# Kernel tuning notes

Measured on AMD Instinct MI355X. Metric: run time of the kernel, lower is better.

The kernel has to match this reference:

```python
import jax, jax.numpy as jnp
import numpy as np

CONF_THRES = 0.3    # from call site: non_max_suppression(pred[0], 0.3)
IOU_THRES = 0.45    # yolov5 default
MAX_NMS = 1000      # candidates entering pairwise NMS
MAX_DET = 300       # padded output detections per image
MAX_WH = 4096.0     # class-offset trick for per-class NMS


def xywh2xyxy(b):
    xy, wh = b[..., :2], b[..., 2:4]
    return jnp.concatenate([xy - wh * 0.5, xy + wh * 0.5], axis=-1)


def box_iou(a, b):
    # a: [K,4], b: [K,4] in xyxy -> iou [K,K]
    area_a = (a[:, 2] - a[:, 0]) * (a[:, 3] - a[:, 1])
    area_b = (b[:, 2] - b[:, 0]) * (b[:, 3] - b[:, 1])
    lt = jnp.maximum(a[:, None, :2], b[None, :, :2])
    rb = jnp.minimum(a[:, None, 2:], b[None, :, 2:])
    wh = jnp.clip(rb - lt, 0.0)
    inter = wh[..., 0] * wh[..., 1]
    return inter / (area_a[:, None] + area_b[None, :] - inter + 1e-7)


def _nms_single(p):
    # p: [N, 5+nc]  (xywh, obj, class scores)
    boxes = xywh2xyxy(p[:, :4])                       # [N,4]
    obj = p[:, 4]
    cls_conf = p[:, 5:] * obj[:, None]                # obj * cls
    cls = jnp.argmax(cls_conf, axis=-1)               # [N] int
    score = jnp.max(cls_conf, axis=-1)                 # [N]
    valid = (obj > CONF_THRES) & (score > CONF_THRES)
    s = jnp.where(valid, score, -jnp.inf)
    top_s, idx = jax.lax.top_k(s, MAX_NMS)            # sorted desc
    b = boxes[idx]                                     # [K,4]
    c = cls[idx]                                       # [K]
    v = top_s > -jnp.inf                               # [K] candidate mask
    # per-class NMS: shift boxes by class id so different classes never overlap
    ob = b + (c.astype(b.dtype) * MAX_WH)[:, None]
    iou = box_iou(ob, ob)                              # [K,K]

    def step(keep, xs):
        i, row = xs
        suppressed = jnp.any(keep & (row > IOU_THRES))
        ki = v[i] & ~suppressed
        return keep.at[i].set(ki), ki

    keep0 = jnp.zeros(MAX_NMS, dtype=bool)
    _, keep = jax.lax.scan(step, keep0, (jnp.arange(MAX_NMS), iou))

    # gather kept detections (score-ordered), pad to MAX_DET
    kscore = jnp.where(keep, top_s, -jnp.inf)
    det_s, det_i = jax.lax.top_k(kscore, MAX_DET)
    det_valid = (det_s > -jnp.inf)[:, None]
    det = jnp.concatenate(
        [b[det_i],                                  # xyxy
         top_s[det_i][:, None],                     # score
         c[det_i].astype(b.dtype)[:, None]],        # class
        axis=-1)                                    # [MAX_DET, 6]
    return jnp.where(det_valid, det, 0.0)


def setup_inputs() -> dict:
    key = jax.random.key(0)
    k1, k2, k3, k4 = jax.random.split(key, 4)
    B, N, NC = 16, 25200, 80
    xy = jax.random.uniform(k1, (B, N, 2), jnp.float32) * 640.0
    wh = jax.random.uniform(k2, (B, N, 2), jnp.float32) * 120.0 + 4.0
    obj = jax.random.uniform(k3, (B, N, 1), jnp.float32)
    cls = jax.random.uniform(k4, (B, N, NC), jnp.float32)
    pred = jnp.concatenate([xy, wh, obj, cls], axis=-1)  # [B,N,85]
    return {"pred": pred}


def reference(pred) -> jnp.ndarray:
    # pred: [B, N, 5+nc] -> detections [B, MAX_DET, 6] (xyxy, conf, cls), zero-padded
    return jax.vmap(_nms_single)(pred)
```

## Files before the change

### kernel.cpp

```cpp
#include <hip/hip_runtime.h>
#include <cstdint>

typedef unsigned int u32;
typedef unsigned long long u64;

#define N_BATCH 16
#define N_ROWS  25200
#define N_FEAT  85
#define N_CLS   80
#define MAX_NMS 1000
#define MAX_DET 300
#define KEY_INVALID 0xFF800000u

#define WS_KEYS    0u
#define WS_CLS     1612800u
#define WS_SELBOX  3225600u
#define WS_SELOB   3487744u
#define WS_SELAREA 3749888u
#define WS_SELSC   3815424u
#define WS_SELCLS  3880960u
#define WS_SELVAL  3946496u
#define WS_GMASK   4012032u

__device__ __forceinline__ u32 score_key(float s) {
  u32 u = __float_as_uint(s);
  u32 o = (u & 0x80000000u) ? ~u : (u | 0x80000000u);
  return ~o;
}

__device__ __forceinline__ u64 shfl_xor_u64(u64 x, int m) {
  u32 lo = (u32)x, hi = (u32)(x >> 32);
  lo = __shfl_xor(lo, m); hi = __shfl_xor(hi, m);
  return ((u64)hi << 32) | lo;
}
__device__ __forceinline__ u64 readlane_u64(u64 x, int lane) {
  u32 lo = (u32)x, hi = (u32)(x >> 32);
  u32 rlo = (u32)__builtin_amdgcn_readlane((int)lo, lane);
  u32 rhi = (u32)__builtin_amdgcn_readlane((int)hi, lane);
  return ((u64)rhi << 32) | rlo;
}

#define KS_CHUNK  32
#define KS_CBYTES (KS_CHUNK * N_FEAT * 4)
#define KS_GRID   1792
#define KS_NCHUNK ((N_BATCH * N_ROWS) / KS_CHUNK)

__device__ __forceinline__ void ks_stage(const float* pred, int c, u32* lbuf,
                                         int wv, int lane) {
  const char* g = (const char*)pred + (size_t)c * KS_CBYTES;
  const int u0 = wv * 170;
  u32* l0 = lbuf + u0 * 4;
  __builtin_amdgcn_global_load_lds(
      (const __attribute__((address_space(1))) u32*)(g + (size_t)(u0 + lane) * 16),
      (__attribute__((address_space(3))) u32*)(l0), 16, 0, 0);
  __builtin_amdgcn_global_load_lds(
      (const __attribute__((address_space(1))) u32*)(g + (size_t)(u0 + 64 + lane) * 16),
      (__attribute__((address_space(3))) u32*)(l0 + 256), 16, 0, 0);
  if (lane < 42)
    __builtin_amdgcn_global_load_lds(
        (const __attribute__((address_space(1))) u32*)(g + (size_t)(u0 + 128 + lane) * 16),
        (__attribute__((address_space(3))) u32*)(l0 + 512), 16, 0, 0);
}

__global__ __launch_bounds__(256) void k_score(const float* __restrict__ pred,
                                               u32* __restrict__ keys,
                                               u32* __restrict__ clsArr) {
  __shared__ __align__(16) u32 sbuf[2][KS_CBYTES / 4];
  const int t = threadIdx.x;
  const int lane = t & 63;
  const int wv = t >> 6;
  const int row = (lane >> 3) + wv * 8;
  const int sub = lane & 7;

  ks_stage(pred, blockIdx.x, sbuf[0], wv, lane);
  ks_stage(pred, blockIdx.x + KS_GRID, sbuf[1], wv, lane);

  int it = 0;
  for (int c = blockIdx.x; c < KS_NCHUNK; c += KS_GRID, ++it) {
    const bool has_next = (c + KS_GRID < KS_NCHUNK);
    if (has_next) asm volatile("s_waitcnt vmcnt(3)" ::: "memory");
    else          asm volatile("s_waitcnt vmcnt(0)" ::: "memory");
    __builtin_amdgcn_sched_barrier(0);
    __builtin_amdgcn_s_barrier();

    const u32* rp = sbuf[it & 1] + row * N_FEAT;
    float obj = __uint_as_float(rp[4]);
    float best = -__builtin_inff();
    int bi = 0;
    const u32* cp = rp + 5 + sub * 10;
    #pragma unroll
    for (int k = 0; k < 10; ++k) {
      float cc = __uint_as_float(cp[k]) * obj;
      if (cc > best) { best = cc; bi = sub * 10 + k; }
    }
    #pragma unroll
    for (int d = 1; d <= 4; d <<= 1) {
      float ob = __shfl_xor(best, d);
      int oj = __shfl_xor(bi, d);
      if (ob > best || (ob == best && oj < bi)) { best = ob; bi = oj; }
    }
    if (sub == 0) {
      bool valid = (obj > 0.3f) && (best > 0.3f);
      float s = valid ? best : -__builtin_inff();
      int gr = c * KS_CHUNK + row;
      keys[gr] = score_key(s);
      clsArr[gr] = (u32)bi;
    }
    __builtin_amdgcn_s_barrier();
    if (c + 2 * KS_GRID < KS_NCHUNK)
      ks_stage(pred, c + 2 * KS_GRID, sbuf[it & 1], wv, lane);
  }
}

#define RPT 25
__global__ __launch_bounds__(1024) void k_select(const float* __restrict__ pred,
    const u32* __restrict__ keys_g, const u32* __restrict__ cls_g,
    float* __restrict__ selBox, float* __restrict__ selOb, float* __restrict__ selArea,
    float* __restrict__ selScore, float* __restrict__ selCls, u32* __restrict__ selValid) {
  extern __shared__ char smem[];
  u32* skeys = (u32*)smem;
  u32* hist  = (u32*)(smem + 102400);
  u32* wsum  = (u32*)(smem + 103424);
  u32* bc    = (u32*)(smem + 103552);
  u64* items = (u64*)(smem + 103584);

  const int b = blockIdx.x;
  const int t = threadIdx.x;
  const int lane = t & 63;
  const int wv = t >> 6;

  {
    uint4* k4 = (uint4*)skeys;
    const uint4* g4 = (const uint4*)(keys_g + b * N_ROWS);
    for (int i = t; i < N_ROWS / 4; i += 1024) k4[i] = g4[i];
  }
  items[t] = 0xFFFFFFFF00000000ull | (u32)t;
  if (t == 0) { bc[0] = 0u; bc[1] = 999u; }
  __syncthreads();

  u32 rk[RPT];
  const int i0 = t * RPT;
  #pragma unroll
  for (int r = 0; r < RPT; ++r) {
    u32 k = skeys[i0 + r];
    rk[r] = (i0 + r < N_ROWS) ? k : 0xFFFFFFFFu;
  }

  for (int lev = 3; lev >= 0; --lev) {
    if (t < 256) hist[t] = 0u;
    __syncthreads();
    const u32 prefix = bc[0];
    const u32 target = bc[1];
    const int sh = lev * 8;
    if (lev == 3) {
      #pragma unroll
      for (int r = 0; r < RPT; ++r) {
        u32 bk = rk[r] >> 24;
        u64 act = __ballot(true);
        while (act) {
          int ldr = __ffsll((unsigned long long)act) - 1;
          u32 lb = __shfl(bk, ldr);
          u64 same = __ballot(bk == lb);
          if (lane == ldr) atomicAdd(&hist[lb], (u32)__popcll(same));
          act &= ~same;
        }
      }
    } else {
      const u32 maskhi = 0xFFFFFFFFu << ((lev + 1) * 8);
      #pragma unroll
      for (int r = 0; r < RPT; ++r) {
        if ((rk[r] & maskhi) == prefix)
          atomicAdd(&hist[(rk[r] >> sh) & 255u], 1u);
      }
    }
    __syncthreads();
    if (t < 64) {
      u32 c0 = hist[t*4], c1 = hist[t*4+1], c2 = hist[t*4+2], c3 = hist[t*4+3];
      u32 s4 = c0 + c1 + c2 + c3;
      u32 inc = s4;
      #pragma unroll
      for (int d = 1; d < 64; d <<= 1) { u32 o = __shfl_up(inc, d); if (lane >= d) inc += o; }
      u32 excl = inc - s4;
      u64 mb = __ballot(inc > target);
      int L = __ffsll((unsigned long long)mb) - 1;
      if (t == L) {
        u32 cum = excl; u32 d = (u32)t * 4u;
        if (cum + c0 <= target) { cum += c0; d++;
          if (cum + c1 <= target) { cum += c1; d++;
            if (cum + c2 <= target) { cum += c2; d++; } } }
        bc[0] = prefix | (d << sh);
        bc[1] = target - cum;
      }
    }
    __syncthreads();
  }
  const u32 T = bc[0];

  u32 c0 = 0, c1 = 0;
  #pragma unroll
  for (int r = 0; r < RPT; ++r) { c0 += (rk[r] < T); c1 += (rk[r] == T); }
  u32 packed = (c0 << 16) | c1;
  u32 inc = packed;
  #pragma unroll
  for (int d = 1; d < 64; d <<= 1) { u32 o = __shfl_up(inc, d); if (lane >= d) inc += o; }
  if (lane == 63) wsum[wv] = inc;
  __syncthreads();
  if (t < 16) {
    u32 v = wsum[t]; u32 iv = v;
    #pragma unroll
    for (int d = 1; d < 16; d <<= 1) { u32 o = __shfl_up(iv, d); if (lane >= d) iv += o; }
    wsum[t] = iv - v;
    if (t == 15) bc[2] = iv;
  }
  __syncthreads();
  u32 excl = inc - packed + wsum[wv];
  u32 total0 = bc[2] >> 16;
  u32 p0 = excl >> 16;
  u32 p1 = total0 + (excl & 0xFFFFu);
  #pragma unroll
  for (int r = 0; r < RPT; ++r) {
    u32 k = rk[r];
    if (k < T)       { items[p0] = ((u64)k << 32) | (u32)(i0 + r); p0++; }
    else if (k == T) { if (p1 < (u32)MAX_NMS) items[p1] = ((u64)k << 32) | (u32)(i0 + r); p1++; }
  }
  __syncthreads();

  u64 v = items[t];
  #pragma unroll
  for (int k = 2; k <= 64; k <<= 1) {
    for (int j = k >> 1; j > 0; j >>= 1) {
      u64 p = shfl_xor_u64(v, j);
      bool keepmin = (((t & k) == 0) == ((t & j) == 0));
      v = (keepmin == (v < p)) ? v : p;
    }
  }
  for (int k = 128; k <= 1024; k <<= 1) {
    for (int j = k >> 1; j >= 64; j >>= 1) {
      items[t] = v;
      __syncthreads();
      u64 p = items[t ^ j];
      bool keepmin = (((t & k) == 0) == ((t & j) == 0));
      v = (keepmin == (v < p)) ? v : p;
      __syncthreads();
    }
    #pragma unroll
    for (int j = 32; j > 0; j >>= 1) {
      u64 p = shfl_xor_u64(v, j);
      bool keepmin = (((t & k) == 0) == ((t & j) == 0));
      v = (keepmin == (v < p)) ? v : p;
    }
  }

  if (t < MAX_NMS) {
    u64 it = v;
    u32 key = (u32)(it >> 32);
    u32 row = (u32)(it & 0xFFFFFFFFu);
    u32 o = ~key;
    u32 sb = (o & 0x80000000u) ? (o ^ 0x80000000u) : ~o;
    float score = __uint_as_float(sb);
    u32 valid = (key != KEY_INVALID) ? 1u : 0u;
    const float* p = pred + ((size_t)b * N_ROWS + row) * N_FEAT;
    float x = p[0], y = p[1], w = p[2], h = p[3];
    float x1 = x - w * 0.5f, y1 = y - h * 0.5f;
    float x2 = x + w * 0.5f, y2 = y + h * 0.5f;
    float cf = (float)cls_g[b * N_ROWS + row];
    float offv = cf * 4096.0f;
    float o0 = x1 + offv, o1 = y1 + offv, o2 = x2 + offv, o3 = y2 + offv;
    float area = (o2 - o0) * (o3 - o1);
    int idx = b * 1024 + t;
    selBox[idx * 4 + 0] = x1; selBox[idx * 4 + 1] = y1;
    selBox[idx * 4 + 2] = x2; selBox[idx * 4 + 3] = y2;
    selOb [idx * 4 + 0] = o0; selOb [idx * 4 + 1] = o1;
    selOb [idx * 4 + 2] = o2; selOb [idx * 4 + 3] = o3;
    selArea[idx] = area;
    selScore[idx] = score;
    selCls[idx] = cf;
    selValid[idx] = valid;
  }
}

__global__ __launch_bounds__(256) void k_mask(const float* __restrict__ selOb,
                                              const float* __restrict__ selArea,
                                              u64* __restrict__ gmask) {
  __shared__ float shob[1024 * 4];
  __shared__ float sharea[1024];
  const int chunk = blockIdx.x;
  const int b = blockIdx.y;
  const int t = threadIdx.x;
  const int lane = t & 63;
  const int wv = t >> 6;
  {
    float4* so4 = (float4*)shob;
    const float4* go4 = (const float4*)(selOb + (size_t)b * 4096);
    for (int i = t; i < 1024; i += 256) so4[i] = go4[i];
    float4* sa4 = (float4*)sharea;
    const float4* ga4 = (const float4*)(selArea + (size_t)b * 1024);
    if (t < 256) sa4[t] = ga4[t];
  }
  __syncthreads();
  const float4* job = (const float4*)shob;
  for (int k = 0; k < 8; ++k) {
    int i = chunk * 32 + wv * 8 + k;
    if (i >= MAX_NMS) break;
    float a0 = shob[i*4+0], a1 = shob[i*4+1], a2 = shob[i*4+2], a3 = shob[i*4+3];
    float aa = sharea[i];
    for (int w = (i >> 6); w < 16; ++w) {
      int j = w * 64 + lane;
      float4 bb = job[j];
      float aj = sharea[j];
      float lt0 = fmaxf(a0, bb.x);
      float lt1 = fmaxf(a1, bb.y);
      float rb0 = fminf(a2, bb.z);
      float rb1 = fminf(a3, bb.w);
      float ww = fmaxf(rb0 - lt0, 0.0f);
      float hh = fmaxf(rb1 - lt1, 0.0f);
      float inter = ww * hh;
      float den = aa + aj - inter + 1e-7f;
      float iou = inter / den;
      u64 bits = __ballot(iou > 0.45f);
      if (lane == 0) gmask[((size_t)b * MAX_NMS + i) * 16 + w] = bits;
    }
  }
}

__global__ __launch_bounds__(256) void k_scan(const u64* __restrict__ gmask,
                                              const u32* __restrict__ selValid,
                                              const float* __restrict__ selBox,
                                              const float* __restrict__ selScore,
                                              const float* __restrict__ selCls,
                                              float* __restrict__ out) {
  extern __shared__ char smem[];
  u64* m = (u64*)smem;
  u64* aw = (u64*)(smem + 128000);
  int* order = (int*)(smem + 128128);
  u32* pcnt = (u32*)(smem + 129328);
  const int b = blockIdx.x;
  const int t = threadIdx.x;
  const int lane = t & 63;
  const int wv = t >> 6;

  {
    const char* g = (const char*)(gmask + (size_t)b * (MAX_NMS * 16));
    for (int u = wv; u < 125; u += 4) {
      __builtin_amdgcn_global_load_lds(
          (const __attribute__((address_space(1))) u32*)(g + (size_t)u * 1024 + (size_t)lane * 16),
          (__attribute__((address_space(3))) u32*)((u32*)m + u * 256), 16, 0, 0);
    }
  }
  for (int s = t; s < 1024; s += 256) {
    u32 vv = (s < MAX_NMS) ? selValid[b * 1024 + s] : 0u;
    u64 bal = __ballot(vv != 0u);
    if ((s & 63) == 0) aw[s >> 6] = bal;
  }
  asm volatile("s_waitcnt vmcnt(0)" ::: "memory");
  __syncthreads();

  if (t < 64) {
    u64 A = (t < 16) ? aw[t] : 0ull;
    int cnt = 0;
    for (int w0 = 0; w0 < 16 && cnt < MAX_DET; ++w0) {
      u64 Aw = readlane_u64(A, w0);
      if (Aw == 0ull) continue;
      int myrow = w0 * 64 + t;
      u64 dm = (myrow < MAX_NMS) ? m[myrow * 16 + w0] : 0ull;
      u32 dml = (u32)dm, dmh = (u32)(dm >> 32);
      u64 keepw = 0ull;
      const int cnt0 = cnt;
      while (Aw != 0ull && cnt < MAX_DET) {
        int bit = __ffsll((unsigned long long)Aw) - 1;
        keepw |= (1ull << bit);
        ++cnt;
        u64 sup = ((u64)(u32)__builtin_amdgcn_readlane((int)dmh, bit) << 32)
                |        (u32)__builtin_amdgcn_readlane((int)dml, bit);
        Aw &= ~sup;
        Aw &= ~(1ull << bit);
      }
      if ((keepw >> t) & 1ull) {
        int rank = (int)__popcll(keepw & ((1ull << t) - 1ull));
        order[cnt0 + rank] = w0 * 64 + t;
      }
      if (cnt >= MAX_DET) break;
      u64 kk = keepw;
      const u64* mr = m + (size_t)w0 * 64 * 16;
      while (kk != 0ull) {
        int b0 = __ffsll((unsigned long long)kk) - 1; kk &= kk - 1;
        int b1 = b0, b2 = b0, b3 = b0;
        if (kk) { b1 = __ffsll((unsigned long long)kk) - 1; kk &= kk - 1;
          if (kk) { b2 = __ffsll((unsigned long long)kk) - 1; kk &= kk - 1;
            if (kk) { b3 = __ffsll((unsigned long long)kk) - 1; kk &= kk - 1; } } }
        if (t < 16) {
          u64 r0 = mr[b0 * 16 + t];
          u64 r1 = mr[b1 * 16 + t];
          u64 r2 = mr[b2 * 16 + t];
          u64 r3 = mr[b3 * 16 + t];
          A &= ~(r0 | r1 | r2 | r3);
        }
      }
    }
    if (t == 0) *pcnt = (u32)cnt;
  }
  __syncthreads();
  int cnt = (int)*pcnt;
  for (int s = t; s < MAX_DET; s += 256) {
    float o0=0,o1=0,o2=0,o3=0,o4=0,o5=0;
    if (s < cnt) {
      int i = order[s];
      int idx = b * 1024 + i;
      o0 = selBox[idx*4+0]; o1 = selBox[idx*4+1];
      o2 = selBox[idx*4+2]; o3 = selBox[idx*4+3];
      o4 = selScore[idx];   o5 = selCls[idx];
    }
    float* op = out + ((size_t)b * MAX_DET + s) * 6;
    op[0]=o0; op[1]=o1; op[2]=o2; op[3]=o3; op[4]=o4; op[5]=o5;
  }
}

extern "C" void kernel_launch(void* const* d_in, const int* in_sizes, int n_in,
                              void* d_out, int out_size, void* d_ws, size_t ws_size,
                              hipStream_t stream) {
  const float* pred = (const float*)d_in[0];
  float* out = (float*)d_out;
  char* ws = (char*)d_ws;
  u32* keys     = (u32*)(ws + WS_KEYS);
  u32* cls      = (u32*)(ws + WS_CLS);
  float* selBox = (float*)(ws + WS_SELBOX);
  float* selOb  = (float*)(ws + WS_SELOB);
  float* selArea= (float*)(ws + WS_SELAREA);
  float* selScore=(float*)(ws + WS_SELSC);
  float* selCls = (float*)(ws + WS_SELCLS);
  u32* selValid = (u32*)(ws + WS_SELVAL);
  u64* gmask    = (u64*)(ws + WS_GMASK);

  k_score<<<KS_GRID, 256, 0, stream>>>(pred, keys, cls);
  k_select<<<N_BATCH, 1024, 111776, stream>>>(pred, keys, cls, selBox, selOb, selArea,
                                              selScore, selCls, selValid);
  k_mask<<<dim3(32, N_BATCH), 256, 0, stream>>>(selOb, selArea, gmask);
  k_scan<<<N_BATCH, 256, 129344, stream>>>(gmask, selValid, selBox, selScore, selCls, out);
}
```

Measured before the change: 108.3 us.

## Fuse four NMS kernels into one persistent kernel with grid barriers

Replaces the score, select, mask and scan launches with one persistent kernel of 256 blocks of 1024 threads. Stages are separated by atomic-counter grid barriers, and a memset resets the counter each call. The aim is to remove per-launch overhead and inter-kernel gaps. In exchange, later stages use only 16 of the 256 blocks while the rest spin, and the scheme depends on all blocks being co-resident; the 129 KB of shared memory per block may limit that.

```diff
diff --git a/kernel.cpp b/kernel.cpp
--- a/kernel.cpp
+++ b/kernel.cpp
@@ -21,6 +21,7 @@
 #define WS_SELCLS  3880960u
 #define WS_SELVAL  3946496u
 #define WS_GMASK   4012032u
+#define WS_BAR     6060032u
 
 __device__ __forceinline__ u32 score_key(float s) {
   u32 u = __float_as_uint(s);
@@ -42,13 +43,14 @@
 
 #define KS_CHUNK  32
 #define KS_CBYTES (KS_CHUNK * N_FEAT * 4)
-#define KS_GRID   1792
 #define KS_NCHUNK ((N_BATCH * N_ROWS) / KS_CHUNK)
+#define MB_NB     256
+#define MB_NT     1024
 
 __device__ __forceinline__ void ks_stage(const float* pred, int c, u32* lbuf,
-                                         int wv, int lane) {
+                                         int gw, int lane) {
   const char* g = (const char*)pred + (size_t)c * KS_CBYTES;
-  const int u0 = wv * 170;
+  const int u0 = gw * 170;
   u32* l0 = lbuf + u0 * 4;
   __builtin_amdgcn_global_load_lds(
       (const __attribute__((address_space(1))) u32*)(g + (size_t)(u0 + lane) * 16),
@@ -62,356 +64,367 @@
         (__attribute__((address_space(3))) u32*)(l0 + 512), 16, 0, 0);
 }
 
-__global__ __launch_bounds__(256) void k_score(const float* __restrict__ pred,
-                                               u32* __restrict__ keys,
-                                               u32* __restrict__ clsArr) {
-  __shared__ __align__(16) u32 sbuf[2][KS_CBYTES / 4];
+__device__ __forceinline__ void grid_barrier(u32* bar, u32 tgt) {
+  __syncthreads();
+  if (threadIdx.x == 0) {
+    __threadfence();
+    __hip_atomic_fetch_add(bar, 1u, __ATOMIC_ACQ_REL, __HIP_MEMORY_SCOPE_AGENT);
+    int spins = 0;
+    while (__hip_atomic_load(bar, __ATOMIC_ACQUIRE, __HIP_MEMORY_SCOPE_AGENT) < tgt) {
+      __builtin_amdgcn_s_sleep(8);
+      if (++spins > 5000000) break;
+    }
+  }
+  __syncthreads();
+}
+
+#define RPT 25
+
+__global__ __launch_bounds__(1024, 4) void k_all(
+    const float* __restrict__ pred, u32* __restrict__ keys, u32* __restrict__ cls_g,
+    float* __restrict__ selBox, float* __restrict__ selOb, float* __restrict__ selArea,
+    float* __restrict__ selScore, float* __restrict__ selCls, u32* __restrict__ selValid,
+    u64* __restrict__ gmask, float* __restrict__ out, u32* __restrict__ bar) {
+  extern __shared__ char smem[];
   const int t = threadIdx.x;
   const int lane = t & 63;
-  const int wv = t >> 6;
-  const int row = (lane >> 3) + wv * 8;
-  const int sub = lane & 7;
-
-  ks_stage(pred, blockIdx.x, sbuf[0], wv, lane);
-  ks_stage(pred, blockIdx.x + KS_GRID, sbuf[1], wv, lane);
-
-  int it = 0;
-  for (int c = blockIdx.x; c < KS_NCHUNK; c += KS_GRID, ++it) {
-    const bool has_next = (c + KS_GRID < KS_NCHUNK);
-    if (has_next) asm volatile("s_waitcnt vmcnt(3)" ::: "memory");
-    else          asm volatile("s_waitcnt vmcnt(0)" ::: "memory");
-    __builtin_amdgcn_sched_barrier(0);
-    __builtin_amdgcn_s_barrier();
-
-    const u32* rp = sbuf[it & 1] + row * N_FEAT;
-    float obj = __uint_as_float(rp[4]);
-    float best = -__builtin_inff();
-    int bi = 0;
-    const u32* cp = rp + 5 + sub * 10;
-    #pragma unroll
-    for (int k = 0; k < 10; ++k) {
-      float cc = __uint_as_float(cp[k]) * obj;
-      if (cc > best) { best = cc; bi = sub * 10 + k; }
-    }
-    #pragma unroll
-    for (int d = 1; d <= 4; d <<= 1) {
-      float ob = __shfl_xor(best, d);
-      int oj = __shfl_xor(bi, d);
-      if (ob > best || (ob == best && oj < bi)) { best = ob; bi = oj; }
-    }
-    if (sub == 0) {
-      bool valid = (obj > 0.3f) && (best > 0.3f);
-      float s = valid ? best : -__builtin_inff();
-      int gr = c * KS_CHUNK + row;
-      keys[gr] = score_key(s);
-      clsArr[gr] = (u32)bi;
-    }
-    __builtin_amdgcn_s_barrier();
-    if (c + 2 * KS_GRID < KS_NCHUNK)
-      ks_stage(pred, c + 2 * KS_GRID, sbuf[it & 1], wv, lane);
+  const int w = t >> 6;
+
+  {
+    const int g = w >> 2;
+    const int gw = w & 3;
+    u32* b0 = (u32*)smem + g * (2 * (KS_CBYTES / 4));
+    u32* b1 = b0 + (KS_CBYTES / 4);
+    const int row = (lane >> 3) + gw * 8;
+    const int sub = lane & 7;
+    const int v = blockIdx.x * 4 + g;
+
+    ks_stage(pred, v, b0, gw, lane);
+    ks_stage(pred, v + 1024, b1, gw, lane);
+
+    for (int it = 0; it < 13; ++it) {
+      const int c = v + it * 1024;
+      const bool active = c < KS_NCHUNK;
+      const bool has_next = (c + 1024) < KS_NCHUNK;
+      if (active) {
+        if (has_next) asm volatile("s_waitcnt vmcnt(3)" ::: "memory");
+        else          asm volatile("s_waitcnt vmcnt(0)" ::: "memory");
+      }
+      __builtin_amdgcn_sched_barrier(0);
+      __builtin_amdgcn_s_barrier();
+      if (active) {
+        const u32* rp = ((it & 1) ? b1 : b0) + row * N_FEAT;
+        float obj = __uint_as_float(rp[4]);
+        float best = -__builtin_inff();
+        int bi = 0;
+        const u32* cp = rp + 5 + sub * 10;
+        #pragma unroll
+        for (int k = 0; k < 10; ++k) {
+          float cc = __uint_as_float(cp[k]) * obj;
+          if (cc > best) { best = cc; bi = sub * 10 + k; }
+        }
+        #pragma unroll
+        for (int d = 1; d <= 4; d <<= 1) {
+          float ob = __shfl_xor(best, d);
+          int oj = __shfl_xor(bi, d);
+          if (ob > best || (ob == best && oj < bi)) { best = ob; bi = oj; }
+        }
+        if (sub == 0) {
+          bool valid = (obj > 0.3f) && (best > 0.3f);
+          float s = valid ? best : -__builtin_inff();
+          int gr = c * KS_CHUNK + row;
+          keys[gr] = score_key(s);
+          cls_g[gr] = (u32)bi;
+        }
+      }
+      __builtin_amdgcn_s_barrier();
+      if (active && (c + 2048) < KS_NCHUNK)
+        ks_stage(pred, c + 2048, (it & 1) ? b1 : b0, gw, lane);
+    }
   }
-}
-
-#define RPT 25
-__global__ __launch_bounds__(1024) void k_select(const float* __restrict__ pred,
-    const u32* __restrict__ keys_g, const u32* __restrict__ cls_g,
-    float* __restrict__ selBox, float* __restrict__ selOb, float* __restrict__ selArea,
-    float* __restrict__ selScore, float* __restrict__ selCls, u32* __restrict__ selValid) {
-  extern __shared__ char smem[];
-  u32* skeys = (u32*)smem;
-  u32* hist  = (u32*)(smem + 102400);
-  u32* wsum  = (u32*)(smem + 103424);
-  u32* bc    = (u32*)(smem + 103552);
-  u64* items = (u64*)(smem + 103584);
-
-  const int b = blockIdx.x;
-  const int t = threadIdx.x;
-  const int lane = t & 63;
-  const int wv = t >> 6;
+  grid_barrier(bar, 256u);
+
+  if (blockIdx.x < N_BATCH) {
+    u32* skeys = (u32*)smem;
+    u32* hist  = (u32*)(smem + 102400);
+    u32* wsum  = (u32*)(smem + 103424);
+    u32* bc    = (u32*)(smem + 103552);
+    u64* items = (u64*)(smem + 103584);
+    const int b = blockIdx.x;
+    const int wv = w;
+    {
+      uint4* k4 = (uint4*)skeys;
+      const uint4* g4 = (const uint4*)(keys + b * N_ROWS);
+      for (int i = t; i < N_ROWS / 4; i += 1024) k4[i] = g4[i];
+    }
+    items[t] = 0xFFFFFFFF00000000ull | (u32)t;
+    if (t == 0) { bc[0] = 0u; bc[1] = 999u; }
+    __syncthreads();
+
+    u32 rk[RPT];
+    const int i0 = t * RPT;
+    #pragma unroll
+    for (int r = 0; r < RPT; ++r) {
+      u32 k = skeys[i0 + r];
+      rk[r] = (i0 + r < N_ROWS) ? k : 0xFFFFFFFFu;
+    }
+
+    for (int lev = 3; lev >= 0; --lev) {
+      if (t < 256) hist[t] = 0u;
+      __syncthreads();
+      const u32 prefix = bc[0];
+      const u32 target = bc[1];
+      const int sh = lev * 8;
+      if (lev == 3) {
+        #pragma unroll
+        for (int r = 0; r < RPT; ++r) {
+          u32 bk = rk[r] >> 24;
+          u64 act = __ballot(true);
+          while (act) {
+            int ldr = __ffsll((unsigned long long)act) - 1;
+            u32 lb = __shfl(bk, ldr);
+            u64 same = __ballot(bk == lb);
+            if (lane == ldr) atomicAdd(&hist[lb], (u32)__popcll(same));
+            act &= ~same;
+          }
+        }
+      } else {
+        const u32 maskhi = 0xFFFFFFFFu << ((lev + 1) * 8);
+        #pragma unroll
+        for (int r = 0; r < RPT; ++r) {
+          if ((rk[r] & maskhi) == prefix)
+            atomicAdd(&hist[(rk[r] >> sh) & 255u], 1u);
+        }
+      }
+      __syncthreads();
+      if (t < 64) {
+        u32 c0 = hist[t*4], c1 = hist[t*4+1], c2 = hist[t*4+2], c3 = hist[t*4+3];
+        u32 s4 = c0 + c1 + c2 + c3;
+        u32 inc = s4;
+        #pragma unroll
+        for (int d = 1; d < 64; d <<= 1) { u32 o = __shfl_up(inc, d); if (lane >= d) inc += o; }
+        u32 excl = inc - s4;
+        u64 mb = __ballot(inc > target);
+        int L = __ffsll((unsigned long long)mb) - 1;
+        if (t == L) {
+          u32 cum = excl; u32 d = (u32)t * 4u;
+          if (cum + c0 <= target) { cum += c0; d++;
+            if (cum + c1 <= target) { cum += c1; d++;
+              if (cum + c2 <= target) { cum += c2; d++; } } }
+          bc[0] = prefix | (d << sh);
+          bc[1] = target - cum;
+        }
+      }
+      __syncthreads();
+    }
+    const u32 T = bc[0];
+
+    u32 c0 = 0, c1 = 0;
+    #pragma unroll
+    for (int r = 0; r < RPT; ++r) { c0 += (rk[r] < T); c1 += (rk[r] == T); }
+    u32 packed = (c0 << 16) | c1;
+    u32 inc = packed;
+    #pragma unroll
+    for (int d = 1; d < 64; d <<= 1) { u32 o = __shfl_up(inc, d); if (lane >= d) inc += o; }
+    if (lane == 63) wsum[wv] = inc;
+    __syncthreads();
+    if (t < 16) {
+      u32 v2 = wsum[t]; u32 iv = v2;
+      #pragma unroll
+      for (int d = 1; d < 16; d <<= 1) { u32 o = __shfl_up(iv, d); if (lane >= d) iv += o; }
+      wsum[t] = iv - v2;
+      if (t == 15) bc[2] = iv;
+    }
+    __syncthreads();
+    u32 excl = inc - packed + wsum[wv];
+    u32 total0 = bc[2] >> 16;
+    u32 p0 = excl >> 16;
+    u32 p1 = total0 + (excl & 0xFFFFu);
+    #pragma unroll
+    for (int r = 0; r < RPT; ++r) {
+      u32 k = rk[r];
+      if (k < T)       { items[p0] = ((u64)k << 32) | (u32)(i0 + r); p0++; }
+      else if (k == T) { if (p1 < (u32)MAX_NMS) items[p1] = ((u64)k << 32) | (u32)(i0 + r); p1++; }
+    }
+    __syncthreads();
+
+    u64 v = items[t];
+    #pragma unroll
+    for (int k = 2; k <= 64; k <<= 1) {
+      for (int j = k >> 1; j > 0; j >>= 1) {
+        u64 p = shfl_xor_u64(v, j);
+        bool keepmin = (((t & k) == 0) == ((t & j) == 0));
+        v = (keepmin == (v < p)) ? v : p;
+      }
+    }
+    for (int k = 128; k <= 1024; k <<= 1) {
+      for (int j = k >> 1; j >= 64; j >>= 1) {
+        items[t] = v;
+        __syncthreads();
+        u64 p = items[t ^ j];
+        bool keepmin = (((t & k) == 0) == ((t & j) == 0));
+        v = (keepmin == (v < p)) ? v : p;
+        __syncthreads();
+      }
+      #pragma unroll
+      for (int j = 32; j > 0; j >>= 1) {
+        u64 p = shfl_xor_u64(v, j);
+        bool keepmin = (((t & k) == 0) == ((t & j) == 0));
+        v = (keepmin == (v < p)) ? v : p;
+      }
+    }
+
+    if (t < MAX_NMS) {
+      u64 it2 = v;
+      u32 key = (u32)(it2 >> 32);
+      u32 row = (u32)(it2 & 0xFFFFFFFFu);
+      u32 o = ~key;
+      u32 sb = (o & 0x80000000u) ? (o ^ 0x80000000u) : ~o;
+      float score = __uint_as_float(sb);
+      u32 valid = (key != KEY_INVALID) ? 1u : 0u;
+      const float* p = pred + ((size_t)b * N_ROWS + row) * N_FEAT;
+      float x = p[0], y = p[1], ww2 = p[2], h = p[3];
+      float x1 = x - ww2 * 0.5f, y1 = y - h * 0.5f;
+      float x2 = x + ww2 * 0.5f, y2 = y + h * 0.5f;
+      float cf = (float)cls_g[b * N_ROWS + row];
+      float offv = cf * 4096.0f;
+      float o0 = x1 + offv, o1 = y1 + offv, o2 = x2 + offv, o3 = y2 + offv;
+      float area = (o2 - o0) * (o3 - o1);
+      int idx = b * 1024 + t;
+      selBox[idx * 4 + 0] = x1; selBox[idx * 4 + 1] = y1;
+      selBox[idx * 4 + 2] = x2; selBox[idx * 4 + 3] = y2;
+      selOb [idx * 4 + 0] = o0; selOb [idx * 4 + 1] = o1;
+      selOb [idx * 4 + 2] = o2; selOb [idx * 4 + 3] = o3;
+      selArea[idx] = area;
+      selScore[idx] = score;
+      selCls[idx] = cf;
+      selValid[idx] = valid;
+    }
+  }
+  grid_barrier(bar, 512u);
 
   {
-    uint4* k4 = (uint4*)skeys;
-    const uint4* g4 = (const uint4*)(keys_g + b * N_ROWS);
-    for (int i = t; i < N_ROWS / 4; i += 1024) k4[i] = g4[i];
+    float* shob = (float*)smem;
+    float* sharea = (float*)(smem + 16384);
+    #pragma unroll
+    for (int pass = 0; pass < 2; ++pass) {
+      const int task = blockIdx.x + 256 * pass;
+      const int chunk = task >> 4;
+      const int bb = task & 15;
+      __syncthreads();
+      ((float4*)shob)[t] = ((const float4*)(selOb + (size_t)bb * 4096))[t];
+      if (t < 256) ((float4*)sharea)[t] = ((const float4*)(selArea + (size_t)bb * 1024))[t];
+      __syncthreads();
+      const float4* job = (const float4*)shob;
+      #pragma unroll
+      for (int k = 0; k < 2; ++k) {
+        int i = chunk * 32 + w * 2 + k;
+        if (i >= MAX_NMS) continue;
+        float a0 = shob[i*4+0], a1 = shob[i*4+1], a2 = shob[i*4+2], a3 = shob[i*4+3];
+        float aa = sharea[i];
+        for (int ww = (i >> 6); ww < 16; ++ww) {
+          int j = ww * 64 + lane;
+          float4 bb4 = job[j];
+          float aj = sharea[j];
+          float lt0 = fmaxf(a0, bb4.x);
+          float lt1 = fmaxf(a1, bb4.y);
+          float rb0 = fminf(a2, bb4.z);
+          float rb1 = fminf(a3, bb4.w);
+          float w2 = fmaxf(rb0 - lt0, 0.0f);
+          float h2 = fmaxf(rb1 - lt1, 0.0f);
+          float inter = w2 * h2;
+          float den = aa + aj - inter + 1e-7f;
+          float iou = inter / den;
+          u64 bits = __ballot(iou > 0.45f);
+          if (lane == 0) gmask[((size_t)bb * MAX_NMS + i) * 16 + ww] = bits;
+        }
+      }
+    }
   }
-  items[t] = 0xFFFFFFFF00000000ull | (u32)t;
-  if (t == 0) { bc[0] = 0u; bc[1] = 999u; }
-  __syncthreads();
-
-  u32 rk[RPT];
-  const int i0 = t * RPT;
-  #pragma unroll
-  for (int r = 0; r < RPT; ++r) {
-    u32 k = skeys[i0 + r];
-    rk[r] = (i0 + r < N_ROWS) ? k : 0xFFFFFFFFu;
-  }
-
-  for (int lev = 3; lev >= 0; --lev) {
-    if (t < 256) hist[t] = 0u;
-    __syncthreads();
-    const u32 prefix = bc[0];
-    const u32 target = bc[1];
-    const int sh = lev * 8;
-    if (lev == 3) {
-      #pragma unroll
-      for (int r = 0; r < RPT; ++r) {
-        u32 bk = rk[r] >> 24;
-        u64 act = __ballot(true);
-        while (act) {
-          int ldr = __ffsll((unsigned long long)act) - 1;
-          u32 lb = __shfl(bk, ldr);
-          u64 same = __ballot(bk == lb);
-          if (lane == ldr) atomicAdd(&hist[lb], (u32)__popcll(same));
-          act &= ~same;
-        }
-      }
-    } else {
-      const u32 maskhi = 0xFFFFFFFFu << ((lev + 1) * 8);
-      #pragma unroll
-      for (int r = 0; r < RPT; ++r) {
-        if ((rk[r] & maskhi) == prefix)
-          atomicAdd(&hist[(rk[r] >> sh) & 255u], 1u);
-      }
-    }
-    __syncthreads();
+  grid_barrier(bar, 768u);
+
+  if (blockIdx.x < N_BATCH) {
+    u64* m = (u64*)smem;
+    u64* aw = (u64*)(smem + 128000);
+    int* order = (int*)(smem + 128128);
+    u32* pcnt = (u32*)(smem + 129328);
+    const int b = blockIdx.x;
+    {
+      const char* g = (const char*)(gmask + (size_t)b * (MAX_NMS * 16));
+      for (int u = w; u < 125; u += 16) {
+        __builtin_amdgcn_global_load_lds(
+            (const __attribute__((address_space(1))) u32*)(g + (size_t)u * 1024 + (size_t)lane * 16),
+            (__attribute__((address_space(3))) u32*)((u32*)m + u * 256), 16, 0, 0);
+      }
+    }
+    {
+      int s = t;
+      u32 vv = (s < MAX_NMS) ? selValid[b * 1024 + s] : 0u;
+      u64 bal = __ballot(vv != 0u);
+      if ((s & 63) == 0) aw[s >> 6] = bal;
+    }
+    asm volatile("s_waitcnt vmcnt(0)" ::: "memory");
+    __syncthreads();
+
     if (t < 64) {
-      u32 c0 = hist[t*4], c1 = hist[t*4+1], c2 = hist[t*4+2], c3 = hist[t*4+3];
-      u32 s4 = c0 + c1 + c2 + c3;
-      u32 inc = s4;
-      #pragma unroll
-      for (int d = 1; d < 64; d <<= 1) { u32 o = __shfl_up(inc, d); if (lane >= d) inc += o; }
-      u32 excl = inc - s4;
-      u64 mb = __ballot(inc > target);
-      int L = __ffsll((unsigned long long)mb) - 1;
-      if (t == L) {
-        u32 cum = excl; u32 d = (u32)t * 4u;
-        if (cum + c0 <= target) { cum += c0; d++;
-          if (cum + c1 <= target) { cum += c1; d++;
-            if (cum + c2 <= target) { cum += c2; d++; } } }
-        bc[0] = prefix | (d << sh);
-        bc[1] = target - cum;
-      }
-    }
-    __syncthreads();
-  }
-  const u32 T = bc[0];
-
-  u32 c0 = 0, c1 = 0;
-  #pragma unroll
-  for (int r = 0; r < RPT; ++r) { c0 += (rk[r] < T); c1 += (rk[r] == T); }
-  u32 packed = (c0 << 16) | c1;
-  u32 inc = packed;
-  #pragma unroll
-  for (int d = 1; d < 64; d <<= 1) { u32 o = __shfl_up(inc, d); if (lane >= d) inc += o; }
-  if (lane == 63) wsum[wv] = inc;
-  __syncthreads();
-  if (t < 16) {
-    u32 v = wsum[t]; u32 iv = v;
-    #pragma unroll
-    for (int d = 1; d < 16; d <<= 1) { u32 o = __shfl_up(iv, d); if (lane >= d) iv += o; }
-    wsum[t] = iv - v;
-    if (t == 15) bc[2] = iv;
-  }
-  __syncthreads();
-  u32 excl = inc - packed + wsum[wv];
-  u32 total0 = bc[2] >> 16;
-  u32 p0 = excl >> 16;
-  u32 p1 = total0 + (excl & 0xFFFFu);
-  #pragma unroll
-  for (int r = 0; r < RPT; ++r) {
-    u32 k = rk[r];
-    if (k < T)       { items[p0] = ((u64)k << 32) | (u32)(i0 + r); p0++; }
-    else if (k == T) { if (p1 < (u32)MAX_NMS) items[p1] = ((u64)k << 32) | (u32)(i0 + r); p1++; }
-  }
-  __syncthreads();
-
-  u64 v = items[t];
-  #pragma unroll
-  for (int k = 2; k <= 64; k <<= 1) {
-    for (int j = k >> 1; j > 0; j >>= 1) {
-      u64 p = shfl_xor_u64(v, j);
-      bool keepmin = (((t & k) == 0) == ((t & j) == 0));
-      v = (keepmin == (v < p)) ? v : p;
-    }
-  }
-  for (int k = 128; k <= 1024; k <<= 1) {
-    for (int j = k >> 1; j >= 64; j >>= 1) {
-      items[t] = v;
-      __syncthreads();
-      u64 p = items[t ^ j];
-      bool keepmin = (((t & k) == 0) == ((t & j) == 0));
-      v = (keepmin == (v < p)) ? v : p;
-      __syncthreads();
-    }
-    #pragma unroll
-    for (int j = 32; j > 0; j >>= 1) {
-      u64 p = shfl_xor_u64(v, j);
-      bool keepmin = (((t & k) == 0) == ((t & j) == 0));
-      v = (keepmin == (v < p)) ? v : p;
-    }
-  }
-
-  if (t < MAX_NMS) {
-    u64 it = v;
-    u32 key = (u32)(it >> 32);
-    u32 row = (u32)(it & 0xFFFFFFFFu);
-    u32 o = ~key;
-    u32 sb = (o & 0x80000000u) ? (o ^ 0x80000000u) : ~o;
-    float score = __uint_as_float(sb);
-    u32 valid = (key != KEY_INVALID) ? 1u : 0u;
-    const float* p = pred + ((size_t)b * N_ROWS + row) * N_FEAT;
-    float x = p[0], y = p[1], w = p[2], h = p[3];
-    float x1 = x - w * 0.5f, y1 = y - h * 0.5f;
-    float x2 = x + w * 0.5f, y2 = y + h * 0.5f;
-    float cf = (float)cls_g[b * N_ROWS + row];
-    float offv = cf * 4096.0f;
-    float o0 = x1 + offv, o1 = y1 + offv, o2 = x2 + offv, o3 = y2 + offv;
-    float area = (o2 - o0) * (o3 - o1);
-    int idx = b * 1024 + t;
-    selBox[idx * 4 + 0] = x1; selBox[idx * 4 + 1] = y1;
-    selBox[idx * 4 + 2] = x2; selBox[idx * 4 + 3] = y2;
-    selOb [idx * 4 + 0] = o0; selOb [idx * 4 + 1] = o1;
-    selOb [idx * 4 + 2] = o2; selOb [idx * 4 + 3] = o3;
-    selArea[idx] = area;
-    selScore[idx] = score;
-    selCls[idx] = cf;
-    selValid[idx] = valid;
-  }
-}
-
-__global__ __launch_bounds__(256) void k_mask(const float* __restrict__ selOb,
-                                              const float* __restrict__ selArea,
-                                              u64* __restrict__ gmask) {
-  __shared__ float shob[1024 * 4];
-  __shared__ float sharea[1024];
-  const int chunk = blockIdx.x;
-  const int b = blockIdx.y;
-  const int t = threadIdx.x;
-  const int lane = t & 63;
-  const int wv = t >> 6;
-  {
-    float4* so4 = (float4*)shob;
-    const float4* go4 = (const float4*)(selOb + (size_t)b * 4096);
-    for (int i = t; i < 1024; i += 256) so4[i] = go4[i];
-    float4* sa4 = (float4*)sharea;
-    const float4* ga4 = (const float4*)(selArea + (size_t)b * 1024);
-    if (t < 256) sa4[t] = ga4[t];
-  }
-  __syncthreads();
-  const float4* job = (const float4*)shob;
-  for (int k = 0; k < 8; ++k) {
-    int i = chunk * 32 + wv * 8 + k;
-    if (i >= MAX_NMS) break;
-    float a0 = shob[i*4+0], a1 = shob[i*4+1], a2 = shob[i*4+2], a3 = shob[i*4+3];
-    float aa = sharea[i];
-    for (int w = (i >> 6); w < 16; ++w) {
-      int j = w * 64 + lane;
-      float4 bb = job[j];
-      float aj = sharea[j];
-      float lt0 = fmaxf(a0, bb.x);
-      float lt1 = fmaxf(a1, bb.y);
-      float rb0 = fminf(a2, bb.z);
-      float rb1 = fminf(a3, bb.w);
-      float ww = fmaxf(rb0 - lt0, 0.0f);
-      float hh = fmaxf(rb1 - lt1, 0.0f);
-      float inter = ww * hh;
-      float den = aa + aj - inter + 1e-7f;
-      float iou = inter / den;
-      u64 bits = __ballot(iou > 0.45f);
-      if (lane == 0) gmask[((size_t)b * MAX_NMS + i) * 16 + w] = bits;
-    }
-  }
-}
-
-__global__ __launch_bounds__(256) void k_scan(const u64* __restrict__ gmask,
-                                              const u32* __restrict__ selValid,
-                                              const float* __restrict__ selBox,
-                                              const float* __restrict__ selScore,
-                                              const float* __restrict__ selCls,
-                                              float* __restrict__ out) {
-  extern __shared__ char smem[];
-  u64* m = (u64*)smem;
-  u64* aw = (u64*)(smem + 128000);
-  int* order = (int*)(smem + 128128);
-  u32* pcnt = (u32*)(smem + 129328);
-  const int b = blockIdx.x;
-  const int t = threadIdx.x;
-  const int lane = t & 63;
-  const int wv = t >> 6;
-
-  {
-    const char* g = (const char*)(gmask + (size_t)b * (MAX_NMS * 16));
-    for (int u = wv; u < 125; u += 4) {
-      __builtin_amdgcn_global_load_lds(
-          (const __attribute__((address_space(1))) u32*)(g + (size_t)u * 1024 + (size_t)lane * 16),
-          (__attribute__((address_space(3))) u32*)((u32*)m + u * 256), 16, 0, 0);
-    }
-  }
-  for (int s = t; s < 1024; s += 256) {
-    u32 vv = (s < MAX_NMS) ? selValid[b * 1024 + s] : 0u;
-    u64 bal = __ballot(vv != 0u);
-    if ((s & 63) == 0) aw[s >> 6] = bal;
-  }
-  asm volatile("s_waitcnt vmcnt(0)" ::: "memory");
-  __syncthreads();
-
-  if (t < 64) {
-    u64 A = (t < 16) ? aw[t] : 0ull;
-    int cnt = 0;
-    for (int w0 = 0; w0 < 16 && cnt < MAX_DET; ++w0) {
-      u64 Aw = readlane_u64(A, w0);
-      if (Aw == 0ull) continue;
-      int myrow = w0 * 64 + t;
-      u64 dm = (myrow < MAX_NMS) ? m[myrow * 16 + w0] : 0ull;
-      u32 dml = (u32)dm, dmh = (u32)(dm >> 32);
-      u64 keepw = 0ull;
-      const int cnt0 = cnt;
-      while (Aw != 0ull && cnt < MAX_DET) {
-        int bit = __ffsll((unsigned long long)Aw) - 1;
-        keepw |= (1ull << bit);
-        ++cnt;
-        u64 sup = ((u64)(u32)__builtin_amdgcn_readlane((int)dmh, bit) << 32)
-                |        (u32)__builtin_amdgcn_readlane((int)dml, bit);
-        Aw &= ~sup;
-        Aw &= ~(1ull << bit);
-      }
-      if ((keepw >> t) & 1ull) {
-        int rank = (int)__popcll(keepw & ((1ull << t) - 1ull));
-        order[cnt0 + rank] = w0 * 64 + t;
-      }
-      if (cnt >= MAX_DET) break;
-      u64 kk = keepw;
-      const u64* mr = m + (size_t)w0 * 64 * 16;
-      while (kk != 0ull) {
-        int b0 = __ffsll((unsigned long long)kk) - 1; kk &= kk - 1;
-        int b1 = b0, b2 = b0, b3 = b0;
-        if (kk) { b1 = __ffsll((unsigned long long)kk) - 1; kk &= kk - 1;
-          if (kk) { b2 = __ffsll((unsigned long long)kk) - 1; kk &= kk - 1;
-            if (kk) { b3 = __ffsll((unsigned long long)kk) - 1; kk &= kk - 1; } } }
-        if (t < 16) {
-          u64 r0 = mr[b0 * 16 + t];
-          u64 r1 = mr[b1 * 16 + t];
-          u64 r2 = mr[b2 * 16 + t];
-          u64 r3 = mr[b3 * 16 + t];
-          A &= ~(r0 | r1 | r2 | r3);
-        }
-      }
-    }
-    if (t == 0) *pcnt = (u32)cnt;
-  }
-  __syncthreads();
-  int cnt = (int)*pcnt;
-  for (int s = t; s < MAX_DET; s += 256) {
-    float o0=0,o1=0,o2=0,o3=0,o4=0,o5=0;
-    if (s < cnt) {
-      int i = order[s];
-      int idx = b * 1024 + i;
-      o0 = selBox[idx*4+0]; o1 = selBox[idx*4+1];
-      o2 = selBox[idx*4+2]; o3 = selBox[idx*4+3];
-      o4 = selScore[idx];   o5 = selCls[idx];
-    }
-    float* op = out + ((size_t)b * MAX_DET + s) * 6;
-    op[0]=o0; op[1]=o1; op[2]=o2; op[3]=o3; op[4]=o4; op[5]=o5;
+      u64 A = (t < 16) ? aw[t] : 0ull;
+      int cnt = 0;
+      for (int w0 = 0; w0 < 16 && cnt < MAX_DET; ++w0) {
+        u64 Aw = readlane_u64(A, w0);
+        if (Aw == 0ull) continue;
+        int myrow = w0 * 64 + t;
+        u64 dm = (myrow < MAX_NMS) ? m[myrow * 16 + w0] : 0ull;
+        u32 dml = (u32)dm, dmh = (u32)(dm >> 32);
+        u64 keepw = 0ull;
+        const int cnt0 = cnt;
+        while (Aw != 0ull && cnt < MAX_DET) {
+          int bit = __ffsll((unsigned long long)Aw) - 1;
+          keepw |= (1ull << bit);
+          ++cnt;
+          u64 sup = ((u64)(u32)__builtin_amdgcn_readlane((int)dmh, bit) << 32)
+                  |        (u32)__builtin_amdgcn_readlane((int)dml, bit);
+          Aw &= ~sup;
+          Aw &= ~(1ull << bit);
+        }
+        if ((keepw >> t) & 1ull) {
+          int rank = (int)__popcll(keepw & ((1ull << t) - 1ull));
+          order[cnt0 + rank] = w0 * 64 + t;
+        }
+        if (cnt >= MAX_DET) break;
+        u64 kk = keepw;
+        const u64* mr = m + (size_t)w0 * 64 * 16;
+        while (kk != 0ull) {
+          int b0 = __ffsll((unsigned long long)kk) - 1; kk &= kk - 1;
+          int b1 = b0, b2 = b0, b3 = b0;
+          if (kk) { b1 = __ffsll((unsigned long long)kk) - 1; kk &= kk - 1;
+            if (kk) { b2 = __ffsll((unsigned long long)kk) - 1; kk &= kk - 1;
+              if (kk) { b3 = __ffsll((unsigned long long)kk) - 1; kk &= kk - 1; } } }
+          if (t < 16) {
+            u64 r0 = mr[b0 * 16 + t];
+            u64 r1 = mr[b1 * 16 + t];
+            u64 r2 = mr[b2 * 16 + t];
+            u64 r3 = mr[b3 * 16 + t];
+            A &= ~(r0 | r1 | r2 | r3);
+          }
+        }
+      }
+      if (t == 0) *pcnt = (u32)cnt;
+    }
+    __syncthreads();
+    int cnt = (int)*pcnt;
+    if (t < MAX_DET) {
+      int s = t;
+      float o0=0,o1=0,o2=0,o3=0,o4=0,o5=0;
+      if (s < cnt) {
+        int i = order[s];
+        int idx = b * 1024 + i;
+        o0 = selBox[idx*4+0]; o1 = selBox[idx*4+1];
+        o2 = selBox[idx*4+2]; o3 = selBox[idx*4+3];
+        o4 = selScore[idx];   o5 = selCls[idx];
+      }
+      float* op = out + ((size_t)b * MAX_DET + s) * 6;
+      op[0]=o0; op[1]=o1; op[2]=o2; op[3]=o3; op[4]=o4; op[5]=o5;
+    }
   }
 }
 
@@ -430,10 +443,9 @@
   float* selCls = (float*)(ws + WS_SELCLS);
   u32* selValid = (u32*)(ws + WS_SELVAL);
   u64* gmask    = (u64*)(ws + WS_GMASK);
-
-  k_score<<<KS_GRID, 256, 0, stream>>>(pred, keys, cls);
-  k_select<<<N_BATCH, 1024, 111776, stream>>>(pred, keys, cls, selBox, selOb, selArea,
-                                              selScore, selCls, selValid);
-  k_mask<<<dim3(32, N_BATCH), 256, 0, stream>>>(selOb, selArea, gmask);
-  k_scan<<<N_BATCH, 256, 129344, stream>>>(gmask, selValid, selBox, selScore, selCls, out);
-}
+  u32* bar      = (u32*)(ws + WS_BAR);
+
+  hipMemsetAsync(bar, 0, 4, stream);
+  k_all<<<MB_NB, MB_NT, 129344, stream>>>(pred, keys, cls, selBox, selOb, selArea,
+                                          selScore, selCls, selValid, gmask, out, bar);
+}
```

Measured after the change: 195.2 us. 1.8x slower.

## Fuse select, IoU mask and scan kernels into one per-image kernel

Applied to the files above, without the earlier changes.

Merges the top-k selection, pairwise IoU bitmask construction and greedy suppression scan into a single kernel with one 1024-thread block per image. Candidate boxes, areas, validity bits and the suppression mask stay in shared memory instead of going through global workspace, and two kernel launches disappear. In exchange the mask computation runs on only 16 blocks rather than a 2D grid, reducing parallelism, and shared memory use grows to about 150KB per block.

```diff
diff --git a/kernel.cpp b/kernel.cpp
--- a/kernel.cpp
+++ b/kernel.cpp
@@ -15,12 +15,8 @@
 #define WS_KEYS    0u
 #define WS_CLS     1612800u
 #define WS_SELBOX  3225600u
-#define WS_SELOB   3487744u
-#define WS_SELAREA 3749888u
 #define WS_SELSC   3815424u
 #define WS_SELCLS  3880960u
-#define WS_SELVAL  3946496u
-#define WS_GMASK   4012032u
 
 __device__ __forceinline__ u32 score_key(float s) {
   u32 u = __float_as_uint(s);
@@ -113,16 +109,22 @@
 }
 
 #define RPT 25
-__global__ __launch_bounds__(1024) void k_select(const float* __restrict__ pred,
+__global__ __launch_bounds__(1024) void k_fused(const float* __restrict__ pred,
     const u32* __restrict__ keys_g, const u32* __restrict__ cls_g,
-    float* __restrict__ selBox, float* __restrict__ selOb, float* __restrict__ selArea,
-    float* __restrict__ selScore, float* __restrict__ selCls, u32* __restrict__ selValid) {
+    float* __restrict__ selBox, float* __restrict__ selScore,
+    float* __restrict__ selCls, float* __restrict__ out) {
   extern __shared__ char smem[];
   u32* skeys = (u32*)smem;
   u32* hist  = (u32*)(smem + 102400);
   u32* wsum  = (u32*)(smem + 103424);
   u32* bc    = (u32*)(smem + 103552);
   u64* items = (u64*)(smem + 103584);
+  float* shob   = (float*)smem;
+  float* sharea = (float*)(smem + 16384);
+  u64* m     = (u64*)(smem + 20480);
+  u64* aw    = (u64*)(smem + 148480);
+  int* order = (int*)(smem + 148608);
+  u32* pcnt  = (u32*)(smem + 149808);
 
   const int b = blockIdx.x;
   const int t = threadIdx.x;
@@ -145,6 +147,7 @@
     u32 k = skeys[i0 + r];
     rk[r] = (i0 + r < N_ROWS) ? k : 0xFFFFFFFFu;
   }
+  __syncthreads();
 
   for (int lev = 3; lev >= 0; --lev) {
     if (t < 256) hist[t] = 0u;
@@ -206,10 +209,10 @@
   if (lane == 63) wsum[wv] = inc;
   __syncthreads();
   if (t < 16) {
-    u32 v = wsum[t]; u32 iv = v;
+    u32 v2 = wsum[t]; u32 iv = v2;
     #pragma unroll
     for (int d = 1; d < 16; d <<= 1) { u32 o = __shfl_up(iv, d); if (lane >= d) iv += o; }
-    wsum[t] = iv - v;
+    wsum[t] = iv - v2;
     if (t == 15) bc[2] = iv;
   }
   __syncthreads();
@@ -251,108 +254,61 @@
     }
   }
 
+  u32 validR = 0;
   if (t < MAX_NMS) {
-    u64 it = v;
-    u32 key = (u32)(it >> 32);
-    u32 row = (u32)(it & 0xFFFFFFFFu);
+    u64 it2 = v;
+    u32 key = (u32)(it2 >> 32);
+    u32 row = (u32)(it2 & 0xFFFFFFFFu);
     u32 o = ~key;
     u32 sb = (o & 0x80000000u) ? (o ^ 0x80000000u) : ~o;
     float score = __uint_as_float(sb);
-    u32 valid = (key != KEY_INVALID) ? 1u : 0u;
+    validR = (key != KEY_INVALID) ? 1u : 0u;
     const float* p = pred + ((size_t)b * N_ROWS + row) * N_FEAT;
-    float x = p[0], y = p[1], w = p[2], h = p[3];
-    float x1 = x - w * 0.5f, y1 = y - h * 0.5f;
-    float x2 = x + w * 0.5f, y2 = y + h * 0.5f;
+    float x = p[0], y = p[1], w2 = p[2], h = p[3];
+    float x1 = x - w2 * 0.5f, y1 = y - h * 0.5f;
+    float x2 = x + w2 * 0.5f, y2 = y + h * 0.5f;
     float cf = (float)cls_g[b * N_ROWS + row];
     float offv = cf * 4096.0f;
     float o0 = x1 + offv, o1 = y1 + offv, o2 = x2 + offv, o3 = y2 + offv;
     float area = (o2 - o0) * (o3 - o1);
+    shob[t * 4 + 0] = o0; shob[t * 4 + 1] = o1;
+    shob[t * 4 + 2] = o2; shob[t * 4 + 3] = o3;
+    sharea[t] = area;
     int idx = b * 1024 + t;
     selBox[idx * 4 + 0] = x1; selBox[idx * 4 + 1] = y1;
     selBox[idx * 4 + 2] = x2; selBox[idx * 4 + 3] = y2;
-    selOb [idx * 4 + 0] = o0; selOb [idx * 4 + 1] = o1;
-    selOb [idx * 4 + 2] = o2; selOb [idx * 4 + 3] = o3;
-    selArea[idx] = area;
     selScore[idx] = score;
     selCls[idx] = cf;
-    selValid[idx] = valid;
-  }
-}
-
-__global__ __launch_bounds__(256) void k_mask(const float* __restrict__ selOb,
-                                              const float* __restrict__ selArea,
-                                              u64* __restrict__ gmask) {
-  __shared__ float shob[1024 * 4];
-  __shared__ float sharea[1024];
-  const int chunk = blockIdx.x;
-  const int b = blockIdx.y;
-  const int t = threadIdx.x;
-  const int lane = t & 63;
-  const int wv = t >> 6;
+  }
   {
-    float4* so4 = (float4*)shob;
-    const float4* go4 = (const float4*)(selOb + (size_t)b * 4096);
-    for (int i = t; i < 1024; i += 256) so4[i] = go4[i];
-    float4* sa4 = (float4*)sharea;
-    const float4* ga4 = (const float4*)(selArea + (size_t)b * 1024);
-    if (t < 256) sa4[t] = ga4[t];
-  }
-  __syncthreads();
-  const float4* job = (const float4*)shob;
-  for (int k = 0; k < 8; ++k) {
-    int i = chunk * 32 + wv * 8 + k;
-    if (i >= MAX_NMS) break;
-    float a0 = shob[i*4+0], a1 = shob[i*4+1], a2 = shob[i*4+2], a3 = shob[i*4+3];
-    float aa = sharea[i];
-    for (int w = (i >> 6); w < 16; ++w) {
-      int j = w * 64 + lane;
-      float4 bb = job[j];
-      float aj = sharea[j];
-      float lt0 = fmaxf(a0, bb.x);
-      float lt1 = fmaxf(a1, bb.y);
-      float rb0 = fminf(a2, bb.z);
-      float rb1 = fminf(a3, bb.w);
-      float ww = fmaxf(rb0 - lt0, 0.0f);
-      float hh = fmaxf(rb1 - lt1, 0.0f);
-      float inter = ww * hh;
-      float den = aa + aj - inter + 1e-7f;
-      float iou = inter / den;
-      u64 bits = __ballot(iou > 0.45f);
-      if (lane == 0) gmask[((size_t)b * MAX_NMS + i) * 16 + w] = bits;
-    }
-  }
-}
-
-__global__ __launch_bounds__(256) void k_scan(const u64* __restrict__ gmask,
-                                              const u32* __restrict__ selValid,
-                                              const float* __restrict__ selBox,
-                                              const float* __restrict__ selScore,
-                                              const float* __restrict__ selCls,
-                                              float* __restrict__ out) {
-  extern __shared__ char smem[];
-  u64* m = (u64*)smem;
-  u64* aw = (u64*)(smem + 128000);
-  int* order = (int*)(smem + 128128);
-  u32* pcnt = (u32*)(smem + 129328);
-  const int b = blockIdx.x;
-  const int t = threadIdx.x;
-  const int lane = t & 63;
-  const int wv = t >> 6;
+    u64 bal = __ballot(validR != 0u);
+    if ((t & 63) == 0) aw[t >> 6] = bal;
+  }
+  __syncthreads();
 
   {
-    const char* g = (const char*)(gmask + (size_t)b * (MAX_NMS * 16));
-    for (int u = wv; u < 125; u += 4) {
-      __builtin_amdgcn_global_load_lds(
-          (const __attribute__((address_space(1))) u32*)(g + (size_t)u * 1024 + (size_t)lane * 16),
-          (__attribute__((address_space(3))) u32*)((u32*)m + u * 256), 16, 0, 0);
-    }
-  }
-  for (int s = t; s < 1024; s += 256) {
-    u32 vv = (s < MAX_NMS) ? selValid[b * 1024 + s] : 0u;
-    u64 bal = __ballot(vv != 0u);
-    if ((s & 63) == 0) aw[s >> 6] = bal;
-  }
-  asm volatile("s_waitcnt vmcnt(0)" ::: "memory");
+    const float4* job = (const float4*)shob;
+    for (int i = wv; i < MAX_NMS; i += 16) {
+      float a0 = shob[i*4+0], a1 = shob[i*4+1], a2 = shob[i*4+2], a3 = shob[i*4+3];
+      float aa = sharea[i];
+      for (int w0 = (i >> 6); w0 < 16; ++w0) {
+        int j = w0 * 64 + lane;
+        float4 bb = job[j];
+        float aj = sharea[j];
+        float lt0 = fmaxf(a0, bb.x);
+        float lt1 = fmaxf(a1, bb.y);
+        float rb0 = fminf(a2, bb.z);
+        float rb1 = fminf(a3, bb.w);
+        float ww = fmaxf(rb0 - lt0, 0.0f);
+        float hh = fmaxf(rb1 - lt1, 0.0f);
+        float inter = ww * hh;
+        float den = aa + aj - inter + 1e-7f;
+        float iou = inter / den;
+        u64 bits = __ballot(iou > 0.45f);
+        if (lane == 0) m[i * 16 + w0] = bits;
+      }
+    }
+  }
   __syncthreads();
 
   if (t < 64) {
@@ -401,7 +357,8 @@
   }
   __syncthreads();
   int cnt = (int)*pcnt;
-  for (int s = t; s < MAX_DET; s += 256) {
+  if (t < MAX_DET) {
+    int s = t;
     float o0=0,o1=0,o2=0,o3=0,o4=0,o5=0;
     if (s < cnt) {
       int i = order[s];
@@ -424,16 +381,10 @@
   u32* keys     = (u32*)(ws + WS_KEYS);
   u32* cls      = (u32*)(ws + WS_CLS);
   float* selBox = (float*)(ws + WS_SELBOX);
-  float* selOb  = (float*)(ws + WS_SELOB);
-  float* selArea= (float*)(ws + WS_SELAREA);
   float* selScore=(float*)(ws + WS_SELSC);
   float* selCls = (float*)(ws + WS_SELCLS);
-  u32* selValid = (u32*)(ws + WS_SELVAL);
-  u64* gmask    = (u64*)(ws + WS_GMASK);
 
   k_score<<<KS_GRID, 256, 0, stream>>>(pred, keys, cls);
-  k_select<<<N_BATCH, 1024, 111776, stream>>>(pred, keys, cls, selBox, selOb, selArea,
-                                              selScore, selCls, selValid);
-  k_mask<<<dim3(32, N_BATCH), 256, 0, stream>>>(selOb, selArea, gmask);
-  k_scan<<<N_BATCH, 256, 129344, stream>>>(gmask, selValid, selBox, selScore, selCls, out);
-}
+  k_fused<<<N_BATCH, 1024, 149824, stream>>>(pred, keys, cls, selBox, selScore,
+                                             selCls, out);
+}
```

Result: slower. 206.1 us (+90.3%).

## Interleave NMS mask rows across waves and split LDS boxes into SoA

Applied to the files above, without the earlier changes.

The IoU mask kernel now assigns rows to waves in a strided, interleaved way across a doubled grid of blocks, instead of giving each block a contiguous chunk of 32 rows. Because each row only computes the upper triangle, contiguous chunks gave blocks very uneven amounts of work, and striding spreads that work more evenly. Box coordinates are also stored in LDS as separate per-coordinate arrays rather than float4s. The cost is that every block reloads the full box set into LDS, and the load count doubles with the larger grid.

```diff
diff --git a/kernel.cpp b/kernel.cpp
--- a/kernel.cpp
+++ b/kernel.cpp
@@ -282,40 +282,32 @@
 __global__ __launch_bounds__(256) void k_mask(const float* __restrict__ selOb,
                                               const float* __restrict__ selArea,
                                               u64* __restrict__ gmask) {
-  __shared__ float shob[1024 * 4];
+  __shared__ float shx1[1024], shy1[1024], shx2[1024], shy2[1024];
   __shared__ float sharea[1024];
-  const int chunk = blockIdx.x;
   const int b = blockIdx.y;
   const int t = threadIdx.x;
   const int lane = t & 63;
   const int wv = t >> 6;
-  {
-    float4* so4 = (float4*)shob;
-    const float4* go4 = (const float4*)(selOb + (size_t)b * 4096);
-    for (int i = t; i < 1024; i += 256) so4[i] = go4[i];
-    float4* sa4 = (float4*)sharea;
-    const float4* ga4 = (const float4*)(selArea + (size_t)b * 1024);
-    if (t < 256) sa4[t] = ga4[t];
-  }
-  __syncthreads();
-  const float4* job = (const float4*)shob;
-  for (int k = 0; k < 8; ++k) {
-    int i = chunk * 32 + wv * 8 + k;
-    if (i >= MAX_NMS) break;
-    float a0 = shob[i*4+0], a1 = shob[i*4+1], a2 = shob[i*4+2], a3 = shob[i*4+3];
+  for (int i = t; i < 1024; i += 256) {
+    float4 v = ((const float4*)(selOb + (size_t)b * 4096))[i];
+    shx1[i] = v.x; shy1[i] = v.y; shx2[i] = v.z; shy2[i] = v.w;
+    sharea[i] = selArea[b * 1024 + i];
+  }
+  __syncthreads();
+  const int gw = blockIdx.x * 4 + wv;
+  for (int i = gw; i < MAX_NMS; i += 256) {
+    float a0 = shx1[i], a1 = shy1[i], a2 = shx2[i], a3 = shy2[i];
     float aa = sharea[i];
     for (int w = (i >> 6); w < 16; ++w) {
       int j = w * 64 + lane;
-      float4 bb = job[j];
-      float aj = sharea[j];
-      float lt0 = fmaxf(a0, bb.x);
-      float lt1 = fmaxf(a1, bb.y);
-      float rb0 = fminf(a2, bb.z);
-      float rb1 = fminf(a3, bb.w);
+      float lt0 = fmaxf(a0, shx1[j]);
+      float lt1 = fmaxf(a1, shy1[j]);
+      float rb0 = fminf(a2, shx2[j]);
+      float rb1 = fminf(a3, shy2[j]);
       float ww = fmaxf(rb0 - lt0, 0.0f);
       float hh = fmaxf(rb1 - lt1, 0.0f);
       float inter = ww * hh;
-      float den = aa + aj - inter + 1e-7f;
+      float den = aa + sharea[j] - inter + 1e-7f;
       float iou = inter / den;
       u64 bits = __ballot(iou > 0.45f);
       if (lane == 0) gmask[((size_t)b * MAX_NMS + i) * 16 + w] = bits;
@@ -434,6 +426,6 @@
   k_score<<<KS_GRID, 256, 0, stream>>>(pred, keys, cls);
   k_select<<<N_BATCH, 1024, 111776, stream>>>(pred, keys, cls, selBox, selOb, selArea,
                                               selScore, selCls, selValid);
-  k_mask<<<dim3(32, N_BATCH), 256, 0, stream>>>(selOb, selArea, gmask);
+  k_mask<<<dim3(64, N_BATCH), 256, 0, stream>>>(selOb, selArea, gmask);
   k_scan<<<N_BATCH, 256, 129344, stream>>>(gmask, selValid, selBox, selScore, selCls, out);
 }
```

Result: faster. 97.79 us (-9.7%).
